# Kernel tuning notes

Measured on AMD Instinct MI355X. Metric: run time of the kernel, lower is better.

The kernel has to match this reference:

```python
import jax, jax.numpy as jnp
import numpy as np

NUM_HEADS = 32
NUM_KV_HEADS = 8
HEAD_DIM = 128
SCALE = 0.08838834764831845  # 1/sqrt(128)
NUM_SEQS = 8
Q_LEN = 256            # new tokens per sequence (uniform cu_seqlens_q)
MAX_PAGES = 128
PAGE_SIZE = 16
BLOCK_SIZE = 32
NUM_PAGES = NUM_SEQS * MAX_PAGES


def setup_inputs() -> dict:
    key = jax.random.key(0)
    ks = jax.random.split(key, 6)
    total = NUM_SEQS * Q_LEN
    q = jax.random.normal(ks[0], (total, NUM_HEADS * HEAD_DIM), dtype=jnp.float32)
    k = jax.random.normal(ks[1], (total, NUM_KV_HEADS * HEAD_DIM), dtype=jnp.float32)
    v = jax.random.normal(ks[2], (total, NUM_KV_HEADS * HEAD_DIM), dtype=jnp.float32)
    k_cache = jax.random.normal(ks[3], (NUM_PAGES, PAGE_SIZE, NUM_KV_HEADS, HEAD_DIM), dtype=jnp.float32)
    v_cache = jax.random.normal(ks[4], (NUM_PAGES, PAGE_SIZE, NUM_KV_HEADS, HEAD_DIM), dtype=jnp.float32)
    page_tables = jnp.arange(NUM_SEQS * MAX_PAGES, dtype=jnp.int32).reshape(NUM_SEQS, MAX_PAGES)
    context_lens = jax.random.randint(ks[5], (NUM_SEQS,), 0, MAX_PAGES * PAGE_SIZE, dtype=jnp.int32)
    return {
        'q': q, 'k': k, 'v': v,
        'k_cache': k_cache, 'v_cache': v_cache,
        'page_tables': page_tables, 'context_lens': context_lens,
        'page_size': PAGE_SIZE, 'block_size': BLOCK_SIZE,
    }


def reference(q, k, v, k_cache, v_cache, page_tables, context_lens, page_size, block_size):
    B, P = page_tables.shape
    S = q.shape[0] // B
    C = P * page_size                      # max cached context per seq
    G = NUM_HEADS // NUM_KV_HEADS          # GQA group size

    qb = q.reshape(B, S, NUM_KV_HEADS, G, HEAD_DIM)
    kb = k.reshape(B, S, NUM_KV_HEADS, HEAD_DIM)
    vb = v.reshape(B, S, NUM_KV_HEADS, HEAD_DIM)

    # page-table gather of cached K/V: [B, P, page_size, nkvh, hd] -> [B, C, nkvh, hd]
    k_ctx = k_cache[page_tables].reshape(B, C, NUM_KV_HEADS, HEAD_DIM)
    v_ctx = v_cache[page_tables].reshape(B, C, NUM_KV_HEADS, HEAD_DIM)

    k_full = jnp.concatenate([k_ctx, kb], axis=1)  # [B, C+S, nkvh, hd]
    v_full = jnp.concatenate([v_ctx, vb], axis=1)

    T = C + S
    t_idx = jnp.arange(T)
    s_idx = jnp.arange(S)
    # cached positions valid iff t < context_len; new positions use block mask
    ctx_valid = t_idx[None, :] < context_lens[:, None]            # [B, T]
    block_ends = (s_idx // block_size + 1) * block_size           # [S]
    new_valid = block_ends[:, None] > (t_idx[None, :] - C)        # [S, T]
    is_ctx = t_idx < C                                            # [T]
    mask = jnp.where(is_ctx[None, None, :], ctx_valid[:, None, :], new_valid[None, :, :])  # [B, S, T]

    # scores: [B, nkvh, G, S, T]
    scores = jnp.einsum('bsngd,btnd->bngst', qb, k_full) * SCALE
    scores = jnp.where(mask[:, None, None, :, :], scores, jnp.float32(-1e30))
    probs = jax.nn.softmax(scores, axis=-1)
    out = jnp.einsum('bngst,btnd->bsngd', probs, v_full)          # [B, S, nkvh, G, hd]
    return out.reshape(B * S, NUM_HEADS * HEAD_DIM)
```

## Files before the change

### kernel.cpp

```cpp
#include <hip/hip_runtime.h>
#include <hip/hip_bf16.h>

#define NUM_HEADS   32
#define NUM_KV_HEADS 8
#define HEAD_DIM    128
#define GQA          4
#define Q_LEN      256
#define MAX_PAGES  128
#define PAGE_SIZE   16
#define SCALE 0.08838834764831845f
#define LOG2E 1.44269504088896340736f
#define RESCALE_THR 8.0f

#define NCH_MAX   36
#define CHUNK_B   16384
#define KSTREAM   ((size_t)NCH_MAX * CHUNK_B)
#define NITEMS    512

typedef __bf16 bf16x8 __attribute__((ext_vector_type(8)));
typedef float  f32x4  __attribute__((ext_vector_type(4)));

union B8 { uint4 u; bf16x8 v; };

__device__ __forceinline__ unsigned f2bf(float x){
    unsigned u = __builtin_bit_cast(unsigned, x);
    return (u + 0x7fffu + ((u >> 16) & 1u)) >> 16;
}
__device__ __forceinline__ unsigned pack2(float lo, float hi){
    return f2bf(lo) | (f2bf(hi) << 16);
}

typedef __attribute__((address_space(3))) unsigned char lds_as3_t;
typedef const __attribute__((address_space(1))) void gas_v;
typedef __attribute__((address_space(3))) void las_v;

#define GLD16(g, l) __builtin_amdgcn_global_load_lds((gas_v*)(g), (las_v*)(l), 16, 0, 0)

#define TRR(dst, base, OFF) asm volatile("ds_read_b64_tr_b16 %0, %1 offset:" OFF \
                                         : "=v"(dst) : "v"(base))

__global__ __launch_bounds__(256) void prep_kernel(
    const float* __restrict__ knew,
    const float* __restrict__ vnew,
    const float* __restrict__ kcache,
    const float* __restrict__ vcache,
    const int*   __restrict__ ptab,
    const int*   __restrict__ ctxlens,
    unsigned char* __restrict__ kimg,
    unsigned char* __restrict__ vimg)
{
    const int ch  = blockIdx.x;
    const int kvh = blockIdx.y;
    const int b   = blockIdx.z;
    const int ctxlen = ctxlens[b];
    const int lim = ctxlen + Q_LEN;
    const int base = ch * 64;
    if (base >= lim) return;

    const int tid  = threadIdx.x;
    const int srow = tid >> 2;
    const int seg  = tid & 3;
    const int t    = base + srow;

    unsigned char* kdst = kimg + (size_t)(b * 8 + kvh) * KSTREAM + (size_t)ch * CHUNK_B;
    unsigned char* vdst = vimg + (size_t)(b * 8 + kvh) * KSTREAM + (size_t)ch * CHUNK_B;
    const int swz    = (srow & 7) << 4;
    const int vbyte0 = (srow >> 2) * 128 + (srow & 3) * 32;

    if (t < lim){
        size_t roff;
        const float *ksrc, *vsrc;
        if (t < ctxlen){
            const int page = ptab[b * MAX_PAGES + (t >> 4)];
            roff = ((size_t)(page * PAGE_SIZE + (t & 15)) * NUM_KV_HEADS + kvh) * HEAD_DIM;
            ksrc = kcache + roff; vsrc = vcache + roff;
        } else {
            roff = ((size_t)(b * Q_LEN + (t - ctxlen)) * NUM_KV_HEADS + kvh) * HEAD_DIM;
            ksrc = knew + roff; vsrc = vnew + roff;
        }
        const float* kr = ksrc + seg * 32;
        const float* vr = vsrc + seg * 32;
        #pragma unroll
        for (int i = 0; i < 4; ++i){
            float4 a  = *(const float4*)(kr + i * 8);
            float4 c4 = *(const float4*)(kr + i * 8 + 4);
            uint4 wv;
            wv.x = pack2(a.x, a.y);  wv.y = pack2(a.z, a.w);
            wv.z = pack2(c4.x, c4.y); wv.w = pack2(c4.z, c4.w);
            *(uint4*)(kdst + srow * 256 + ((seg * 64 + i * 16) ^ swz)) = wv;
        }
        #pragma unroll
        for (int db = 0; db < 2; ++db){
            const float4 a0 = *(const float4*)(vr + db * 16 + 0);
            const float4 a1 = *(const float4*)(vr + db * 16 + 4);
            const float4 a2 = *(const float4*)(vr + db * 16 + 8);
            const float4 a3 = *(const float4*)(vr + db * 16 + 12);
            uint4 w0, w1;
            w0.x = pack2(a0.x, a0.y); w0.y = pack2(a0.z, a0.w);
            w0.z = pack2(a1.x, a1.y); w0.w = pack2(a1.z, a1.w);
            w1.x = pack2(a2.x, a2.y); w1.y = pack2(a2.z, a2.w);
            w1.z = pack2(a3.x, a3.y); w1.w = pack2(a3.z, a3.w);
            const int dbk = seg * 2 + db;
            *(uint4*)(vdst + dbk * 2048 + vbyte0)      = w0;
            *(uint4*)(vdst + dbk * 2048 + vbyte0 + 16) = w1;
        }
    } else {
        const uint4 z = {0u, 0u, 0u, 0u};
        #pragma unroll
        for (int i = 0; i < 4; ++i)
            *(uint4*)(kdst + srow * 256 + ((seg * 64 + i * 16) ^ swz)) = z;
        #pragma unroll
        for (int db = 0; db < 2; ++db){
            const int dbk = seg * 2 + db;
            *(uint4*)(vdst + dbk * 2048 + vbyte0)      = z;
            *(uint4*)(vdst + dbk * 2048 + vbyte0 + 16) = z;
        }
    }
}

__global__ __launch_bounds__(256, 2) void attn_kernel(
    const float* __restrict__ q,
    const int*   __restrict__ ctxlens,
    float*       __restrict__ out,
    const unsigned char* __restrict__ kimg,
    const unsigned char* __restrict__ vimg)
{
    __shared__ __align__(16) unsigned char lds[65536];

    const int tid  = threadIdx.x;
    const int w    = tid >> 6;
    const int lane = tid & 63;
    const int hh   = lane >> 4;
    const int cq   = lane & 15;

    const unsigned ldsb3 = (unsigned)(unsigned long long)(lds_as3_t*)(&lds[0]);

    const int item0 = blockIdx.x;

    const int b   = item0 & 7;
    const int kvh = (item0 >> 3) & 7;
    const int s32 = 7 - (item0 >> 6);

    const int s0 = s32 * 32;
    const int ctxlen = ctxlens[b];
    const int vlim = ctxlen + (s32 + 1) * 32;
    const int nch  = (vlim + 63) >> 6;
    const int hq = kvh * GQA + w;

    const unsigned char* kstream = kimg + (size_t)(b * 8 + kvh) * KSTREAM;
    const unsigned char* vstream = vimg + (size_t)(b * 8 + kvh) * KSTREAM;

    #define STAGE(CH, PB) do { \
        const unsigned char* kg_ = kstream + (size_t)(CH) * CHUNK_B + (w * 4096 + lane * 16); \
        const unsigned char* vg_ = vstream + (size_t)(CH) * CHUNK_B + (w * 4096 + lane * 16); \
        _Pragma("unroll") \
        for (int i_ = 0; i_ < 4; ++i_){ \
            GLD16(kg_ + i_ * 1024, lds + (PB) * CHUNK_B + w * 4096 + i_ * 1024); \
            GLD16(vg_ + i_ * 1024, lds + 32768 + (PB) * CHUNK_B + w * 4096 + i_ * 1024); \
        } \
    } while (0)

    STAGE(0, 0);

    B8 qf[2][4];
    #pragma unroll
    for (int u = 0; u < 2; ++u){
        const float* qrow = q + (size_t)(b * Q_LEN + s0 + u * 16 + cq) * (NUM_HEADS * HEAD_DIM)
                              + hq * HEAD_DIM;
        #pragma unroll
        for (int c = 0; c < 4; ++c){
            const float4 f0 = *(const float4*)(qrow + c * 32 + 8 * hh);
            const float4 f1 = *(const float4*)(qrow + c * 32 + 8 * hh + 4);
            const float sc = SCALE * LOG2E;
            qf[u][c].u.x = pack2(f0.x * sc, f0.y * sc);
            qf[u][c].u.y = pack2(f0.z * sc, f0.w * sc);
            qf[u][c].u.z = pack2(f1.x * sc, f1.y * sc);
            qf[u][c].u.w = pack2(f1.z * sc, f1.w * sc);
        }
    }

    f32x4 acc[2][8] = {};
    float mrun[2] = {-1e30f, -1e30f};
    float lp[2]   = {0.f, 0.f};

    for (int ch = 0; ch < nch; ++ch){
        const int pb = ch & 1;

        asm volatile("s_waitcnt lgkmcnt(0)" ::: "memory");
        __builtin_amdgcn_s_barrier();
        __builtin_amdgcn_sched_barrier(0);
        if (ch + 1 < nch) {
            STAGE(ch + 1, pb ^ 1);
            __builtin_amdgcn_sched_barrier(0);
            asm volatile("s_waitcnt vmcnt(8)" ::: "memory");
        } else {
            asm volatile("s_waitcnt vmcnt(0)" ::: "memory");
        }
        __builtin_amdgcn_sched_barrier(0);

        const int base = ch * 64;
        const unsigned kb = (unsigned)(pb * CHUNK_B);

        __builtin_amdgcn_s_setprio(1);
        f32x4 st[2][4] = {};
        #pragma unroll
        for (int c = 0; c < 4; ++c){
            #pragma unroll
            for (int tf = 0; tf < 4; ++tf){
                const int trow = tf * 16 + cq;
                const unsigned byte = kb + trow * 256 + ((c * 64 + hh * 16) ^ ((trow & 7) << 4));
                B8 kf; kf.u = *(const uint4*)(lds + byte);
                st[0][tf] = __builtin_amdgcn_mfma_f32_16x16x32_bf16(kf.v, qf[0][c].v, st[0][tf], 0, 0, 0);
                st[1][tf] = __builtin_amdgcn_mfma_f32_16x16x32_bf16(kf.v, qf[1][c].v, st[1][tf], 0, 0, 0);
            }
        }
        __builtin_amdgcn_s_setprio(0);

        const unsigned trb = ldsb3 + 32768u + (unsigned)(pb * CHUNK_B) + (unsigned)(hh * 128 + cq * 8);
        unsigned long long v00,v01,v02,v03,v04,v05,v06,v07,v08,v09,v10,v11,v12,v13,v14,v15;
        unsigned long long v16,v17,v18,v19,v20,v21,v22,v23,v24,v25,v26,v27,v28,v29,v30,v31;
        __builtin_amdgcn_sched_barrier(0);
        TRR(v00, trb, "0");     TRR(v01, trb, "512");
        TRR(v02, trb, "2048");  TRR(v03, trb, "2560");
        TRR(v04, trb, "4096");  TRR(v05, trb, "4608");
        TRR(v06, trb, "6144");  TRR(v07, trb, "6656");
        TRR(v08, trb, "8192");  TRR(v09, trb, "8704");
        TRR(v10, trb, "10240"); TRR(v11, trb, "10752");
        TRR(v12, trb, "12288"); TRR(v13, trb, "12800");
        TRR(v14, trb, "14336"); TRR(v15, trb, "14848");
        TRR(v16, trb, "1024");  TRR(v17, trb, "1536");
        TRR(v18, trb, "3072");  TRR(v19, trb, "3584");
        TRR(v20, trb, "5120");  TRR(v21, trb, "5632");
        TRR(v22, trb, "7168");  TRR(v23, trb, "7680");
        TRR(v24, trb, "9216");  TRR(v25, trb, "9728");
        TRR(v26, trb, "11264"); TRR(v27, trb, "11776");
        TRR(v28, trb, "13312"); TRR(v29, trb, "13824");
        TRR(v30, trb, "15360"); TRR(v31, trb, "15872");
        __builtin_amdgcn_sched_barrier(0);

        B8 af[2][2];
        const bool interior = (base + 64 <= vlim);
        #pragma unroll
        for (int u = 0; u < 2; ++u){
            float p[4][4];
            float pml = -1e30f;
            if (interior){
                #pragma unroll
                for (int tf = 0; tf < 4; ++tf){
                    #pragma unroll
                    for (int r = 0; r < 4; ++r){
                        const float s = st[u][tf][r];
                        p[tf][r] = s;
                        pml = fmaxf(pml, s);
                    }
                }
            } else {
                #pragma unroll
                for (int tf = 0; tf < 4; ++tf){
                    #pragma unroll
                    for (int r = 0; r < 4; ++r){
                        const int t = base + tf * 16 + hh * 4 + r;
                        const float s = (t < vlim) ? st[u][tf][r] : -1e30f;
                        p[tf][r] = s;
                        pml = fmaxf(pml, s);
                    }
                }
            }
            if (!__all(pml <= mrun[u] + RESCALE_THR)){
                float pm = fmaxf(pml, __shfl_xor(pml, 16));
                pm = fmaxf(pm, __shfl_xor(pm, 32));
                const float mnew  = fmaxf(mrun[u], pm);
                const float alpha = __builtin_amdgcn_exp2f(mrun[u] - mnew);
                mrun[u] = mnew;
                lp[u] *= alpha;
                float a4[4];
                #pragma unroll
                for (int r = 0; r < 4; ++r) a4[r] = __shfl(alpha, hh * 20 + r);
                #pragma unroll
                for (int dc = 0; dc < 8; ++dc){
                    #pragma unroll
                    for (int r = 0; r < 4; ++r) acc[u][dc][r] *= a4[r];
                }
            }
            const float m = mrun[u];
            float rsum = 0.f;
            #pragma unroll
            for (int tf = 0; tf < 4; ++tf){
                #pragma unroll
                for (int r = 0; r < 4; ++r){
                    const float e = __builtin_amdgcn_exp2f(p[tf][r] - m);
                    p[tf][r] = e;
                    rsum += e;
                }
            }
            lp[u] += rsum;

            unsigned pk01[4], pk23[4];
            #pragma unroll
            for (int tf = 0; tf < 4; ++tf){
                pk01[tf] = pack2(p[tf][0], p[tf][1]);
                pk23[tf] = pack2(p[tf][2], p[tf][3]);
            }
            af[u][0].u.x = pk01[0]; af[u][0].u.y = pk23[0]; af[u][0].u.z = pk01[1]; af[u][0].u.w = pk23[1];
            af[u][1].u.x = pk01[2]; af[u][1].u.y = pk23[2]; af[u][1].u.z = pk01[3]; af[u][1].u.w = pk23[3];
        }

        {
            asm volatile("s_waitcnt lgkmcnt(0)" ::: "memory");
            __builtin_amdgcn_sched_barrier(0);
            __builtin_amdgcn_s_setprio(1);
            B8 vf;
            #define PVM(VA, VB, KK, DC) \
                vf.u.x=(unsigned)(VA); vf.u.y=(unsigned)((VA)>>32); \
                vf.u.z=(unsigned)(VB); vf.u.w=(unsigned)((VB)>>32); \
                acc[0][DC] = __builtin_amdgcn_mfma_f32_16x16x32_bf16(af[0][KK].v, vf.v, acc[0][DC], 0, 0, 0); \
                acc[1][DC] = __builtin_amdgcn_mfma_f32_16x16x32_bf16(af[1][KK].v, vf.v, acc[1][DC], 0, 0, 0);
            PVM(v00, v01, 0, 0)  PVM(v02, v03, 0, 1)  PVM(v04, v05, 0, 2)  PVM(v06, v07, 0, 3)
            PVM(v08, v09, 0, 4)  PVM(v10, v11, 0, 5)  PVM(v12, v13, 0, 6)  PVM(v14, v15, 0, 7)
            PVM(v16, v17, 1, 0)  PVM(v18, v19, 1, 1)  PVM(v20, v21, 1, 2)  PVM(v22, v23, 1, 3)
            PVM(v24, v25, 1, 4)  PVM(v26, v27, 1, 5)  PVM(v28, v29, 1, 6)  PVM(v30, v31, 1, 7)
            #undef PVM
            __builtin_amdgcn_s_setprio(0);
        }
    }

    #pragma unroll
    for (int u = 0; u < 2; ++u){
        float l = lp[u];
        l += __shfl_xor(l, 16);
        l += __shfl_xor(l, 32);
        const float li = 1.0f / l;
        float li4[4];
        #pragma unroll
        for (int r = 0; r < 4; ++r) li4[r] = __shfl(li, hh * 20 + r);
        #pragma unroll
        for (int dc = 0; dc < 8; ++dc){
            #pragma unroll
            for (int r = 0; r < 4; ++r){
                const int so = s0 + u * 16 + hh * 4 + r;
                out[(size_t)(b * Q_LEN + so) * (NUM_HEADS * HEAD_DIM) + hq * HEAD_DIM + dc * 16 + cq]
                    = acc[u][dc][r] * li4[r];
            }
        }
    }
    #undef STAGE
}

extern "C" void kernel_launch(void* const* d_in, const int* in_sizes, int n_in,
                              void* d_out, int out_size, void* d_ws, size_t ws_size,
                              hipStream_t stream) {
    const float* q  = (const float*)d_in[0];
    const float* k  = (const float*)d_in[1];
    const float* v  = (const float*)d_in[2];
    const float* kc = (const float*)d_in[3];
    const float* vc = (const float*)d_in[4];
    const int*   pt = (const int*)d_in[5];
    const int*   cl = (const int*)d_in[6];
    float* o = (float*)d_out;

    unsigned char* kimg = (unsigned char*)d_ws + 256;
    unsigned char* vimg = kimg + (size_t)64 * KSTREAM;

    prep_kernel<<<dim3(NCH_MAX, 8, 8), 256, 0, stream>>>(k, v, kc, vc, pt, cl, kimg, vimg);
    attn_kernel<<<NITEMS, 256, 0, stream>>>(q, cl, o, kimg, vimg);
}
```

Before: 113.4 us.

## Load K tiles directly into registers and stage only V in LDS

K fragments for each chunk now go straight from global memory into a register array (kf[4][4]). The next chunk's K is prefetched into registers after the V transpose reads, so K no longer passes through LDS. LDS shrinks from 64KB to 32KB, holding only double-buffered V, and the K image swizzle in the prep kernel is removed because it is no longer needed. The trade is that every wave loads the whole K chunk, so global/L2 traffic for K goes up fourfold. It also adds about 64 live VGPRs, which risks spills under launch_bounds(256,2).

```diff
diff --git a/kernel.cpp b/kernel.cpp
--- a/kernel.cpp
+++ b/kernel.cpp
@@ -64,7 +64,6 @@
 
     unsigned char* kdst = kimg + (size_t)(b * 8 + kvh) * KSTREAM + (size_t)ch * CHUNK_B;
     unsigned char* vdst = vimg + (size_t)(b * 8 + kvh) * KSTREAM + (size_t)ch * CHUNK_B;
-    const int swz    = (srow & 7) << 4;
     const int vbyte0 = (srow >> 2) * 128 + (srow & 3) * 32;
 
     if (t < lim){
@@ -87,7 +86,7 @@
             uint4 wv;
             wv.x = pack2(a.x, a.y);  wv.y = pack2(a.z, a.w);
             wv.z = pack2(c4.x, c4.y); wv.w = pack2(c4.z, c4.w);
-            *(uint4*)(kdst + srow * 256 + ((seg * 64 + i * 16) ^ swz)) = wv;
+            *(uint4*)(kdst + srow * 256 + seg * 64 + i * 16) = wv;
         }
         #pragma unroll
         for (int db = 0; db < 2; ++db){
@@ -108,7 +107,7 @@
         const uint4 z = {0u, 0u, 0u, 0u};
         #pragma unroll
         for (int i = 0; i < 4; ++i)
-            *(uint4*)(kdst + srow * 256 + ((seg * 64 + i * 16) ^ swz)) = z;
+            *(uint4*)(kdst + srow * 256 + seg * 64 + i * 16) = z;
         #pragma unroll
         for (int db = 0; db < 2; ++db){
             const int dbk = seg * 2 + db;
@@ -125,7 +124,7 @@
     const unsigned char* __restrict__ kimg,
     const unsigned char* __restrict__ vimg)
 {
-    __shared__ __align__(16) unsigned char lds[65536];
+    __shared__ __align__(16) unsigned char lds[32768];
 
     const int tid  = threadIdx.x;
     const int w    = tid >> 6;
@@ -136,7 +135,6 @@
     const unsigned ldsb3 = (unsigned)(unsigned long long)(lds_as3_t*)(&lds[0]);
 
     const int item0 = blockIdx.x;
-
     const int b   = item0 & 7;
     const int kvh = (item0 >> 3) & 7;
     const int s32 = 7 - (item0 >> 6);
@@ -149,18 +147,30 @@
 
     const unsigned char* kstream = kimg + (size_t)(b * 8 + kvh) * KSTREAM;
     const unsigned char* vstream = vimg + (size_t)(b * 8 + kvh) * KSTREAM;
-
-    #define STAGE(CH, PB) do { \
-        const unsigned char* kg_ = kstream + (size_t)(CH) * CHUNK_B + (w * 4096 + lane * 16); \
+    const unsigned char* klane   = kstream + (cq * 256 + hh * 16);
+
+    #define STAGE_V(CH, PB) do { \
         const unsigned char* vg_ = vstream + (size_t)(CH) * CHUNK_B + (w * 4096 + lane * 16); \
         _Pragma("unroll") \
         for (int i_ = 0; i_ < 4; ++i_){ \
-            GLD16(kg_ + i_ * 1024, lds + (PB) * CHUNK_B + w * 4096 + i_ * 1024); \
-            GLD16(vg_ + i_ * 1024, lds + 32768 + (PB) * CHUNK_B + w * 4096 + i_ * 1024); \
+            GLD16(vg_ + i_ * 1024, lds + (PB) * 16384 + w * 4096 + i_ * 1024); \
         } \
     } while (0)
 
-    STAGE(0, 0);
+    B8 kf[4][4];
+    #define KLOAD(CH) do { \
+        const unsigned char* kc_ = klane + (size_t)(CH) * CHUNK_B; \
+        _Pragma("unroll") \
+        for (int tf_ = 0; tf_ < 4; ++tf_){ \
+            _Pragma("unroll") \
+            for (int c_ = 0; c_ < 4; ++c_){ \
+                kf[tf_][c_].u = *(const uint4*)(kc_ + tf_ * 4096 + c_ * 64); \
+            } \
+        } \
+    } while (0)
+
+    KLOAD(0);
+    STAGE_V(0, 0);
 
     B8 qf[2][4];
     #pragma unroll
@@ -190,16 +200,15 @@
         __builtin_amdgcn_s_barrier();
         __builtin_amdgcn_sched_barrier(0);
         if (ch + 1 < nch) {
-            STAGE(ch + 1, pb ^ 1);
+            STAGE_V(ch + 1, pb ^ 1);
             __builtin_amdgcn_sched_barrier(0);
-            asm volatile("s_waitcnt vmcnt(8)" ::: "memory");
+            asm volatile("s_waitcnt vmcnt(4)" ::: "memory");
         } else {
             asm volatile("s_waitcnt vmcnt(0)" ::: "memory");
         }
         __builtin_amdgcn_sched_barrier(0);
 
         const int base = ch * 64;
-        const unsigned kb = (unsigned)(pb * CHUNK_B);
 
         __builtin_amdgcn_s_setprio(1);
         f32x4 st[2][4] = {};
@@ -207,16 +216,13 @@
         for (int c = 0; c < 4; ++c){
             #pragma unroll
             for (int tf = 0; tf < 4; ++tf){
-                const int trow = tf * 16 + cq;
-                const unsigned byte = kb + trow * 256 + ((c * 64 + hh * 16) ^ ((trow & 7) << 4));
-                B8 kf; kf.u = *(const uint4*)(lds + byte);
-                st[0][tf] = __builtin_amdgcn_mfma_f32_16x16x32_bf16(kf.v, qf[0][c].v, st[0][tf], 0, 0, 0);
-                st[1][tf] = __builtin_amdgcn_mfma_f32_16x16x32_bf16(kf.v, qf[1][c].v, st[1][tf], 0, 0, 0);
+                st[0][tf] = __builtin_amdgcn_mfma_f32_16x16x32_bf16(kf[tf][c].v, qf[0][c].v, st[0][tf], 0, 0, 0);
+                st[1][tf] = __builtin_amdgcn_mfma_f32_16x16x32_bf16(kf[tf][c].v, qf[1][c].v, st[1][tf], 0, 0, 0);
             }
         }
         __builtin_amdgcn_s_setprio(0);
 
-        const unsigned trb = ldsb3 + 32768u + (unsigned)(pb * CHUNK_B) + (unsigned)(hh * 128 + cq * 8);
+        const unsigned trb = ldsb3 + (unsigned)(pb * 16384) + (unsigned)(hh * 128 + cq * 8);
         unsigned long long v00,v01,v02,v03,v04,v05,v06,v07,v08,v09,v10,v11,v12,v13,v14,v15;
         unsigned long long v16,v17,v18,v19,v20,v21,v22,v23,v24,v25,v26,v27,v28,v29,v30,v31;
         __builtin_amdgcn_sched_barrier(0);
@@ -238,6 +244,8 @@
         TRR(v30, trb, "15360"); TRR(v31, trb, "15872");
         __builtin_amdgcn_sched_barrier(0);
 
+        if (ch + 1 < nch) KLOAD(ch + 1);
+
         B8 af[2][2];
         const bool interior = (base + 64 <= vlim);
         #pragma unroll
@@ -343,7 +351,8 @@
             }
         }
     }
-    #undef STAGE
+    #undef STAGE_V
+    #undef KLOAD
 }
 
 extern "C" void kernel_launch(void* const* d_in, const int* in_sizes, int n_in,
```

After: 280.4 us. 2.47x slower.

## Stage K/V chunks through registers instead of direct global-to-LDS loads

Applied to the files above, without the earlier changes.

Replaces the direct global_load_lds double-buffered staging with a register-staged pipeline. The next chunk is loaded into eight uint4 registers while the current one is computed, then written to LDS at the top of the following iteration. An extra barrier is added after the LDS write. This moves the load latency into the compute phase, but costs more VGPRs, adds ds_write traffic and a second barrier per chunk, and makes the LDS write wait on the global load at the start of each iteration.

```diff
diff --git a/kernel.cpp b/kernel.cpp
--- a/kernel.cpp
+++ b/kernel.cpp
@@ -31,10 +31,6 @@
 }
 
 typedef __attribute__((address_space(3))) unsigned char lds_as3_t;
-typedef const __attribute__((address_space(1))) void gas_v;
-typedef __attribute__((address_space(3))) void las_v;
-
-#define GLD16(g, l) __builtin_amdgcn_global_load_lds((gas_v*)(g), (las_v*)(l), 16, 0, 0)
 
 #define TRR(dst, base, OFF) asm volatile("ds_read_b64_tr_b16 %0, %1 offset:" OFF \
                                          : "=v"(dst) : "v"(base))
@@ -147,20 +143,30 @@
     const int nch  = (vlim + 63) >> 6;
     const int hq = kvh * GQA + w;
 
-    const unsigned char* kstream = kimg + (size_t)(b * 8 + kvh) * KSTREAM;
-    const unsigned char* vstream = vimg + (size_t)(b * 8 + kvh) * KSTREAM;
-
-    #define STAGE(CH, PB) do { \
-        const unsigned char* kg_ = kstream + (size_t)(CH) * CHUNK_B + (w * 4096 + lane * 16); \
-        const unsigned char* vg_ = vstream + (size_t)(CH) * CHUNK_B + (w * 4096 + lane * 16); \
-        _Pragma("unroll") \
-        for (int i_ = 0; i_ < 4; ++i_){ \
-            GLD16(kg_ + i_ * 1024, lds + (PB) * CHUNK_B + w * 4096 + i_ * 1024); \
-            GLD16(vg_ + i_ * 1024, lds + 32768 + (PB) * CHUNK_B + w * 4096 + i_ * 1024); \
-        } \
+    const unsigned char* kstream = kimg + (size_t)(b * 8 + kvh) * KSTREAM + (w * 4096 + lane * 16);
+    const unsigned char* vstream = vimg + (size_t)(b * 8 + kvh) * KSTREAM + (w * 4096 + lane * 16);
+
+    uint4 sr0, sr1, sr2, sr3, sr4, sr5, sr6, sr7;
+
+    #define SLOAD(CH) do { \
+        const unsigned char* kg_ = kstream + (size_t)(CH) * CHUNK_B; \
+        const unsigned char* vg_ = vstream + (size_t)(CH) * CHUNK_B; \
+        sr0 = *(const uint4*)(kg_);          sr1 = *(const uint4*)(kg_ + 1024); \
+        sr2 = *(const uint4*)(kg_ + 2048);   sr3 = *(const uint4*)(kg_ + 3072); \
+        sr4 = *(const uint4*)(vg_);          sr5 = *(const uint4*)(vg_ + 1024); \
+        sr6 = *(const uint4*)(vg_ + 2048);   sr7 = *(const uint4*)(vg_ + 3072); \
     } while (0)
 
-    STAGE(0, 0);
+    #define SWRITE(PB) do { \
+        unsigned char* kb_ = lds + (PB) * CHUNK_B + w * 4096 + lane * 16; \
+        unsigned char* vb_ = lds + 32768 + (PB) * CHUNK_B + w * 4096 + lane * 16; \
+        *(uint4*)(kb_)        = sr0;  *(uint4*)(kb_ + 1024) = sr1; \
+        *(uint4*)(kb_ + 2048) = sr2;  *(uint4*)(kb_ + 3072) = sr3; \
+        *(uint4*)(vb_)        = sr4;  *(uint4*)(vb_ + 1024) = sr5; \
+        *(uint4*)(vb_ + 2048) = sr6;  *(uint4*)(vb_ + 3072) = sr7; \
+    } while (0)
+
+    SLOAD(0);
 
     B8 qf[2][4];
     #pragma unroll
@@ -189,13 +195,12 @@
         asm volatile("s_waitcnt lgkmcnt(0)" ::: "memory");
         __builtin_amdgcn_s_barrier();
         __builtin_amdgcn_sched_barrier(0);
-        if (ch + 1 < nch) {
-            STAGE(ch + 1, pb ^ 1);
-            __builtin_amdgcn_sched_barrier(0);
-            asm volatile("s_waitcnt vmcnt(8)" ::: "memory");
-        } else {
-            asm volatile("s_waitcnt vmcnt(0)" ::: "memory");
-        }
+        SWRITE(pb);
+        __builtin_amdgcn_sched_barrier(0);
+        if (ch + 1 < nch) SLOAD(ch + 1);
+        __builtin_amdgcn_sched_barrier(0);
+        asm volatile("s_waitcnt lgkmcnt(0)" ::: "memory");
+        __builtin_amdgcn_s_barrier();
         __builtin_amdgcn_sched_barrier(0);
 
         const int base = ch * 64;
@@ -343,7 +348,8 @@
             }
         }
     }
-    #undef STAGE
+    #undef SLOAD
+    #undef SWRITE
 }
 
 extern "C" void kernel_launch(void* const* d_in, const int* in_sizes, int n_in,
```

Measured after the change: 118.9 us. 4.9% more time.
